# Kernel optimization log

Hardware: AMD Instinct MI355X
Metric: run time of the kernel (lower is better)

Reference implementation:

```python
import jax, jax.numpy as jnp
import numpy as np

B, IMG, TXT = 1, 2048, 256
D_MODEL = 2048
HEADS, HEAD_DIM = 16, 128
INNER = HEADS * HEAD_DIM
EPS = 1e-5
SCALE = HEAD_DIM ** -0.5


def _rmsnorm(x, w):
    # normalize over last dim (head_dim)
    return (x * jax.lax.rsqrt(jnp.mean(x * x, axis=-1, keepdims=True) + EPS)) * w


def _rope(x, cos, sin):
    # x: (B, S, H, D); cos/sin: (S, D) with pairwise-repeated freqs (interleaved convention)
    c = cos[None, :, None, :]
    s = sin[None, :, None, :]
    x1 = x[..., 0::2]
    x2 = x[..., 1::2]
    rot = jnp.stack([-x2, x1], axis=-1).reshape(x.shape)
    return x * c + rot * s


def setup_inputs() -> dict:
    key = jax.random.key(0)
    ks = jax.random.split(key, 12)
    sc_in = D_MODEL ** -0.5
    sc_inner = INNER ** -0.5
    inp = {
        'hidden_states': jax.random.normal(ks[0], (B, IMG, D_MODEL), jnp.float32),
        'encoder_hidden_states': jax.random.normal(ks[1], (B, TXT, D_MODEL), jnp.float32),
    }
    # RoPE tables over the joint (text + image) sequence, interleaved pair layout
    pos = jnp.arange(TXT + IMG, dtype=jnp.float32)
    inv = 1.0 / (10000.0 ** (jnp.arange(0, HEAD_DIM, 2, dtype=jnp.float32) / HEAD_DIM))
    freqs = pos[:, None] * inv[None, :]
    freqs = jnp.repeat(freqs, 2, axis=-1)  # (S, HEAD_DIM)
    inp['freqs_cos'] = jnp.cos(freqs)
    inp['freqs_sin'] = jnp.sin(freqs)
    # parameters (stored (in, out))
    inp['Wqkv'] = jax.random.normal(ks[2], (D_MODEL, 3 * INNER), jnp.float32) * sc_in
    inp['Wqkv_add'] = jax.random.normal(ks[3], (D_MODEL, 3 * INNER), jnp.float32) * sc_in
    inp['b_qkv_add'] = jax.random.normal(ks[4], (3 * INNER,), jnp.float32) * 0.01
    inp['norm_q_w'] = jnp.ones((HEAD_DIM,), jnp.float32)
    inp['norm_k_w'] = jnp.ones((HEAD_DIM,), jnp.float32)
    inp['norm_aq_w'] = jnp.ones((HEAD_DIM,), jnp.float32)
    inp['norm_ak_w'] = jnp.ones((HEAD_DIM,), jnp.float32)
    inp['Wout'] = jax.random.normal(ks[5], (INNER, D_MODEL), jnp.float32) * sc_inner
    inp['b_out'] = jax.random.normal(ks[6], (D_MODEL,), jnp.float32) * 0.01
    inp['Wadd_out'] = jax.random.normal(ks[7], (INNER, D_MODEL), jnp.float32) * sc_inner
    inp['b_add_out'] = jax.random.normal(ks[8], (D_MODEL,), jnp.float32) * 0.01
    return inp


def reference(hidden_states, encoder_hidden_states, freqs_cos, freqs_sin,
              Wqkv, Wqkv_add, b_qkv_add, norm_q_w, norm_k_w, norm_aq_w, norm_ak_w,
              Wout, b_out, Wadd_out, b_add_out):
    b, s_img, _ = hidden_states.shape
    s_txt = encoder_hidden_states.shape[1]

    # fused QKV projection (image stream), chunk q/k/v, unflatten heads
    qkv = hidden_states @ Wqkv  # (B, IMG, 3*INNER)
    q, k, v = jnp.split(qkv, 3, axis=-1)
    q = _rmsnorm(q.reshape(b, s_img, HEADS, HEAD_DIM), norm_q_w)
    k = _rmsnorm(k.reshape(b, s_img, HEADS, HEAD_DIM), norm_k_w)
    v = v.reshape(b, s_img, HEADS, HEAD_DIM)

    # fused QKV projection (text stream, with bias)
    eqkv = encoder_hidden_states @ Wqkv_add + b_qkv_add
    eq, ek, ev = jnp.split(eqkv, 3, axis=-1)
    eq = _rmsnorm(eq.reshape(b, s_txt, HEADS, HEAD_DIM), norm_aq_w)
    ek = _rmsnorm(ek.reshape(b, s_txt, HEADS, HEAD_DIM), norm_ak_w)
    ev = ev.reshape(b, s_txt, HEADS, HEAD_DIM)

    # joint [text; image] concatenation, then RoPE on joint Q/K
    jq = jnp.concatenate([eq, q], axis=1)
    jk = jnp.concatenate([ek, k], axis=1)
    jv = jnp.concatenate([ev, v], axis=1)
    jq = _rope(jq, freqs_cos, freqs_sin)
    jk = _rope(jk, freqs_cos, freqs_sin)

    # non-causal scaled dot-product attention, layout (B, S, H, D)
    scores = jnp.einsum('bqhd,bkhd->bhqk', jq, jk) * SCALE
    probs = jax.nn.softmax(scores, axis=-1)
    out = jnp.einsum('bhqk,bkhd->bqhd', probs, jv)  # (B, S_joint, H, D)
    out = out.reshape(b, s_txt + s_img, INNER)

    enc_out = out[:, :s_txt]
    img_out = out[:, s_txt:]
    img_out = img_out @ Wout + b_out
    enc_out = enc_out @ Wadd_out + b_add_out
    return (img_out, enc_out)
```

## Files before the change

### kernel.cpp

```cpp
#include <hip/hip_runtime.h>
#include <stdint.h>

#define HEADS 16
#define HD 128
#define S_TXT 256
#define S_IMG 2048
#define S_ALL 2304
#define DMODEL 2048
#define N_QKV 6144
#define INNER 2048
#define ATT_EPS 1e-5f
#define ATT_SCALE 0.08838834764831845f
#define LOG2E 1.4426950408889634f
#define MBOUND 16.5f
#define QT_N 18
#define TPS 18

typedef __attribute__((ext_vector_type(8))) __bf16 bf16x8;
typedef __attribute__((ext_vector_type(4))) float f32x4;
typedef __attribute__((ext_vector_type(4))) uint32_t u32x4;

__device__ __forceinline__ uint16_t f2bf(float f) {
  union { float f; uint32_t u; } v; v.f = f;
  uint32_t r = (v.u + 0x7FFF + ((v.u >> 16) & 1)) >> 16;
  return (uint16_t)r;
}
__device__ __forceinline__ float bf2f(uint16_t h) {
  union { float f; uint32_t u; } v; v.u = ((uint32_t)h) << 16;
  return v.f;
}
__device__ __forceinline__ uint32_t cvt_pk_bf16(float lo, float hi) {
  uint32_t r;
  asm("v_cvt_pk_bf16_f32 %0, %1, %2" : "=v"(r) : "v"(lo), "v"(hi));
  return r;
}
__device__ __forceinline__ float fexp2(float x) {
#if __has_builtin(__builtin_amdgcn_exp2f)
  return __builtin_amdgcn_exp2f(x);
#else
  return __expf(x * 0.69314718055994531f);
#endif
}

__device__ __forceinline__ void async_cp16(const void* g, void* l) {
  __builtin_amdgcn_global_load_lds(
      (const __attribute__((address_space(1))) void*)g,
      (__attribute__((address_space(3))) void*)l, 16, 0, 0);
}

__global__ __launch_bounds__(256) void k_cvt2(
    const float* __restrict__ s0, uint16_t* __restrict__ d0, int n40,
    const float* __restrict__ s1, uint16_t* __restrict__ d1, int n41) {
  const float* src; uint16_t* dst; int n4, bid, nb;
  if (blockIdx.x < 1024) { src = s0; dst = d0; n4 = n40; bid = blockIdx.x; nb = 1024; }
  else { src = s1; dst = d1; n4 = n41; bid = blockIdx.x - 1024; nb = 128; }
  int i = bid * 256 + threadIdx.x;
  int stride = nb * 256;
  for (; i < n4; i += stride) {
    float4 v = ((const float4*)src)[i];
    uint2 o;
    o.x = cvt_pk_bf16(v.x, v.y);
    o.y = cvt_pk_bf16(v.z, v.w);
    ((uint2*)dst)[i] = o;
  }
}

__global__ __launch_bounds__(256) void k_cvt_t4(
    const float* __restrict__ s0, uint16_t* __restrict__ d0,
    const float* __restrict__ s1, uint16_t* __restrict__ d1,
    const float* __restrict__ s2, uint16_t* __restrict__ d2,
    const float* __restrict__ s3, uint16_t* __restrict__ d3) {
  __shared__ float t[64][65];
  int b = blockIdx.x;
  const float* src; uint16_t* dst; int R, C, tb;
  if (b < 3072)      { src = s0; dst = d0; R = DMODEL; C = N_QKV;  tb = b; }
  else if (b < 6144) { src = s1; dst = d1; R = DMODEL; C = N_QKV;  tb = b - 3072; }
  else if (b < 7168) { src = s2; dst = d2; R = INNER;  C = DMODEL; tb = b - 6144; }
  else               { src = s3; dst = d3; R = INNER;  C = DMODEL; tb = b - 7168; }
  int ntr = R >> 6;
  int tr = tb % ntr, tc = tb / ntr;
  int tid = threadIdx.x;
  int rr = tid >> 4, c4 = (tid & 15) * 4;
#pragma unroll
  for (int j = 0; j < 4; ++j) {
    int r = rr + j * 16;
    float4 v = *(const float4*)&src[(size_t)(tr * 64 + r) * C + tc * 64 + c4];
    *(float4*)&t[r][c4] = v;
  }
  __syncthreads();
  int cc = tid >> 4, r4 = (tid & 15) * 4;
#pragma unroll
  for (int j = 0; j < 4; ++j) {
    int c = cc + j * 16;
    uint2 o;
    o.x = cvt_pk_bf16(t[r4 + 0][c], t[r4 + 1][c]);
    o.y = cvt_pk_bf16(t[r4 + 2][c], t[r4 + 3][c]);
    *(uint2*)&dst[(size_t)(tc * 64 + c) * R + tr * 64 + r4] = o;
  }
}

__global__ __launch_bounds__(512, 1) void k_gemm2(
    const uint16_t* __restrict__ A0, const uint16_t* __restrict__ B0,
    const float* __restrict__ bias0, uint16_t* __restrict__ C0,
    const uint16_t* __restrict__ A1, const uint16_t* __restrict__ B1,
    const float* __restrict__ bias1, uint16_t* __restrict__ C1,
    int seg0_tiles, int N, int K) {
  __shared__ __align__(16) char lds[2 * 65536];
  int bn = blockIdx.x, bm = blockIdx.y;
  const uint16_t* A; const uint16_t* B; const float* bias; uint16_t* C; int mrow;
  if (bm < seg0_tiles) { A = A0; B = B0; bias = bias0; C = C0; mrow = bm * 256; }
  else { A = A1; B = B1; bias = bias1; C = C1; mrow = (bm - seg0_tiles) * 256; }
  int tid = threadIdx.x, lane = tid & 63, w = tid >> 6;
  int g = lane >> 4, li = lane & 15;
  int wm = w >> 2, wn = w & 3;
  const int NKI = K / 64;

  int rowin = lane >> 3;
  int csrc = (lane & 7) ^ rowin;

  auto stage = [&](int t, char* buf) {
    int kt = t * 64;
#pragma unroll
    for (int j = 0; j < 4; ++j) {
      int r = w * 4 + j;
      int tr = r * 8 + rowin;
      async_cp16(A + (size_t)(mrow + tr) * K + kt + 8 * csrc, buf + r * 1024);
    }
#pragma unroll
    for (int j = 0; j < 4; ++j) {
      int r = w * 4 + j;
      int tr = r * 8 + rowin;
      async_cp16(B + (size_t)(bn * 256 + tr) * K + kt + 8 * csrc, buf + 32768 + r * 1024);
    }
  };

  f32x4 acc[8][4] = {};

  stage(0, lds);
  asm volatile("s_waitcnt vmcnt(0)" ::: "memory");
  __builtin_amdgcn_s_barrier();
  asm volatile("" ::: "memory");

  for (int t = 0; t < NKI; ++t) {
    const char* cur = lds + (t & 1) * 65536;
    if (t + 1 < NKI) stage(t + 1, lds + ((t + 1) & 1) * 65536);

#pragma unroll
    for (int kk = 0; kk < 2; ++kk) {
      bf16x8 af[8], bfv[4];
#pragma unroll
      for (int mi = 0; mi < 8; ++mi) {
        int row = wm * 128 + mi * 16 + li;
        int ch = (kk * 4 + g) ^ (row & 7);
        af[mi] = __builtin_bit_cast(bf16x8, *(const u32x4*)(cur + row * 128 + ch * 16));
      }
#pragma unroll
      for (int ni = 0; ni < 4; ++ni) {
        int row = wn * 64 + ni * 16 + li;
        int ch = (kk * 4 + g) ^ (row & 7);
        bfv[ni] = __builtin_bit_cast(bf16x8, *(const u32x4*)(cur + 32768 + row * 128 + ch * 16));
      }
      __builtin_amdgcn_s_setprio(1);
#pragma unroll
      for (int mi = 0; mi < 8; ++mi)
#pragma unroll
        for (int ni = 0; ni < 4; ++ni)
          acc[mi][ni] = __builtin_amdgcn_mfma_f32_16x16x32_bf16(af[mi], bfv[ni], acc[mi][ni], 0, 0, 0);
      __builtin_amdgcn_s_setprio(0);
    }

    if (t + 1 < NKI) {
      asm volatile("s_waitcnt vmcnt(0)" ::: "memory");
      __builtin_amdgcn_s_barrier();
      asm volatile("" ::: "memory");
    }
  }

#pragma unroll
  for (int mi = 0; mi < 8; ++mi) {
#pragma unroll
    for (int ni = 0; ni < 4; ++ni) {
      int col = bn * 256 + wn * 64 + ni * 16 + li;
      float bv = bias ? bias[col] : 0.0f;
#pragma unroll
      for (int i = 0; i < 4; ++i) {
        int r = mrow + wm * 128 + mi * 16 + 4 * g + i;
        C[(size_t)r * N + col] = f2bf(acc[mi][ni][i] + bv);
      }
    }
  }
}

__global__ __launch_bounds__(256, 4) void k_gemmO(
    const uint16_t* __restrict__ A0, const uint16_t* __restrict__ B0,
    const float* __restrict__ bias0, float* __restrict__ C0,
    const uint16_t* __restrict__ A1, const uint16_t* __restrict__ B1,
    const float* __restrict__ bias1, float* __restrict__ C1,
    int seg0_tiles, int N, int K) {
  __shared__ __align__(16) char lds[4 * 8192];
  int bn = blockIdx.x, bm = blockIdx.y;
  const uint16_t* A; const uint16_t* B; const float* bias; float* C; int mrow;
  if (bm < seg0_tiles) { A = A0; B = B0; bias = bias0; C = C0; mrow = bm * 128; }
  else { A = A1; B = B1; bias = bias1; C = C1; mrow = (bm - seg0_tiles) * 128; }
  int tid = threadIdx.x, lane = tid & 63, w = tid >> 6;
  int g = lane >> 4, li = lane & 15;
  int wm = w >> 1, wn = w & 1;
  const int NKT = K / 32;

  int rowin = lane >> 2;
  int csrc = (lane & 3) ^ (rowin & 3);

  auto stage = [&](int t, int buf) {
    int kt = t * 32;
#pragma unroll
    for (int j = 0; j < 2; ++j) {
      int r = w * 2 + j;
      int tr = r * 16 + rowin;
      async_cp16(A + (size_t)(mrow + tr) * K + kt + 8 * csrc, lds + buf * 8192 + r * 1024);
    }
#pragma unroll
    for (int j = 0; j < 2; ++j) {
      int r = w * 2 + j;
      int tr = r * 16 + rowin;
      async_cp16(B + (size_t)(bn * 128 + tr) * K + kt + 8 * csrc, lds + 16384 + buf * 8192 + r * 1024);
    }
  };

  f32x4 acc[4][4] = {};
  stage(0, 0);
  asm volatile("s_waitcnt vmcnt(0)" ::: "memory");
  __builtin_amdgcn_s_barrier();
  asm volatile("" ::: "memory");

  for (int t = 0; t < NKT; ++t) {
    int cur = t & 1;
    bool pre = (t + 1 < NKT);
    if (pre) stage(t + 1, cur ^ 1);
    const char* Ac = lds + cur * 8192;
    const char* Bc = lds + 16384 + cur * 8192;

    bf16x8 af[4], bfv[4];
#pragma unroll
    for (int mi = 0; mi < 4; ++mi) {
      int row = wm * 64 + mi * 16 + li;
      af[mi] = __builtin_bit_cast(bf16x8, *(const u32x4*)(Ac + row * 64 + (g ^ (row & 3)) * 16));
    }
#pragma unroll
    for (int ni = 0; ni < 4; ++ni) {
      int row = wn * 64 + ni * 16 + li;
      bfv[ni] = __builtin_bit_cast(bf16x8, *(const u32x4*)(Bc + row * 64 + (g ^ (row & 3)) * 16));
    }
    __builtin_amdgcn_s_setprio(1);
#pragma unroll
    for (int mi = 0; mi < 4; ++mi)
#pragma unroll
      for (int ni = 0; ni < 4; ++ni)
        acc[mi][ni] = __builtin_amdgcn_mfma_f32_16x16x32_bf16(af[mi], bfv[ni], acc[mi][ni], 0, 0, 0);
    __builtin_amdgcn_s_setprio(0);

    if (pre) asm volatile("s_waitcnt vmcnt(0)" ::: "memory");
    __builtin_amdgcn_s_barrier();
    asm volatile("" ::: "memory");
  }

#pragma unroll
  for (int mi = 0; mi < 4; ++mi) {
#pragma unroll
    for (int ni = 0; ni < 4; ++ni) {
      int col = bn * 128 + wn * 64 + ni * 16 + li;
      float bv = bias[col];
#pragma unroll
      for (int i = 0; i < 4; ++i) {
        int r = mrow + wm * 64 + mi * 16 + 4 * g + i;
        C[(size_t)r * N + col] = acc[mi][ni][i] + bv;
      }
    }
  }
}

__global__ __launch_bounds__(256) void k_postvt(
    const uint16_t* __restrict__ qkv_img, const uint16_t* __restrict__ qkv_txt,
    const float* __restrict__ fcos, const float* __restrict__ fsin,
    const float* __restrict__ wq, const float* __restrict__ wk,
    const float* __restrict__ waq, const float* __restrict__ wak,
    uint16_t* __restrict__ Qo, uint16_t* __restrict__ Ko, uint16_t* __restrict__ VTo) {
  __shared__ uint16_t Vl[64][136];
  if (blockIdx.x < S_ALL) {
    int s = blockIdx.x;
    const uint16_t* row = (s < S_TXT) ? qkv_txt + (size_t)s * N_QKV
                                      : qkv_img + (size_t)(s - S_TXT) * N_QKV;
    const float* wqp = (s < S_TXT) ? waq : wq;
    const float* wkp = (s < S_TXT) ? wak : wk;
    int lane = threadIdx.x & 63, w = threadIdx.x >> 6;
    int h = w * 4 + (lane >> 4);
    int d0 = (lane & 15) * 8;
    float cs[8], sn[8];
#pragma unroll
    for (int j = 0; j < 8; ++j) {
      cs[j] = fcos[s * HD + d0 + j];
      sn[j] = fsin[s * HD + d0 + j];
    }
#pragma unroll
    for (int part = 0; part < 2; ++part) {
      const uint16_t* src = row + part * INNER + h * HD + d0;
      u32x4 raw = *(const u32x4*)src;
      const uint16_t* rp = (const uint16_t*)&raw;
      float x[8], ss = 0.f;
#pragma unroll
      for (int j = 0; j < 8; ++j) { x[j] = bf2f(rp[j]); ss += x[j] * x[j]; }
      ss += __shfl_xor(ss, 1); ss += __shfl_xor(ss, 2);
      ss += __shfl_xor(ss, 4); ss += __shfl_xor(ss, 8);
      float rn = rsqrtf(ss * (1.0f / HD) + ATT_EPS);
      const float* wp = part ? wkp : wqp;
#pragma unroll
      for (int j = 0; j < 8; ++j) x[j] = x[j] * rn * wp[d0 + j];
      float y[8];
#pragma unroll
      for (int j = 0; j < 8; j += 2) {
        y[j]     = x[j] * cs[j] - x[j + 1] * sn[j];
        y[j + 1] = x[j + 1] * cs[j + 1] + x[j] * sn[j + 1];
      }
      float sc = part ? 1.0f : (ATT_SCALE * LOG2E);
      uint16_t ov[8];
#pragma unroll
      for (int j = 0; j < 8; ++j) ov[j] = f2bf(y[j] * sc);
      uint16_t* dst = (part ? Ko : Qo) + ((size_t)h * S_ALL + s) * HD + d0;
      *(u32x4*)dst = *(const u32x4*)ov;
    }
  } else {
    int b = blockIdx.x - S_ALL;
    int st = b % 36, h = b / 36;
    int s0 = st * 64;
    const uint16_t* base = (s0 < S_TXT) ? qkv_txt + (size_t)s0 * N_QKV
                                        : qkv_img + (size_t)(s0 - S_TXT) * N_QKV;
    base += 2 * INNER + h * HD;
    int tid = threadIdx.x;
#pragma unroll
    for (int it = 0; it < 4; ++it) {
      int idx = it * 256 + tid;
      int r = idx >> 4, c = idx & 15;
      *(u32x4*)&Vl[r][c * 8] = *(const u32x4*)(base + (size_t)r * N_QKV + c * 8);
    }
    __syncthreads();
#pragma unroll
    for (int it = 0; it < 4; ++it) {
      int idx = it * 256 + tid;
      int d = idx >> 3, sc = (idx & 7) * 8;
      uint16_t tmp[8];
#pragma unroll
      for (int j = 0; j < 8; ++j) tmp[j] = Vl[sc + j][d];
      *(u32x4*)&VTo[((size_t)h * HD + d) * S_ALL + s0 + sc] = *(const u32x4*)tmp;
    }
  }
}

__global__ __launch_bounds__(256, 3) void k_attn(
    const uint16_t* __restrict__ Qg, const uint16_t* __restrict__ Kg,
    const uint16_t* __restrict__ VTg,
    uint16_t* __restrict__ part0, uint16_t* __restrict__ part1,
    uint16_t* __restrict__ part2, uint16_t* __restrict__ part3,
    float* __restrict__ lsumP) {
  __shared__ __align__(16) char Kt[2][8192];
  __shared__ __align__(16) char Vt[2][8192];
  __shared__ __align__(16) uint16_t Pl[4][32 * 40];

  int b0 = blockIdx.x;
  int bid = (b0 & 7) * 144 + (b0 >> 3);
  int h = bid / 72, r6 = bid % 72, sp = r6 / 18, qt = r6 % 18;
  int tid = threadIdx.x, lane = tid & 63, w = tid >> 6;
  int g = lane >> 4, li = lane & 15;

  const uint16_t* Kh = Kg + (size_t)h * S_ALL * HD;
  const uint16_t* Vh = VTg + (size_t)h * HD * S_ALL;
  uint16_t* po = (sp & 2) ? ((sp & 1) ? part3 : part2) : ((sp & 1) ? part1 : part0);
  po += ((size_t)(h * QT_N + qt) * 128 + w * 32) * 128;

  int qbase = qt * 128 + w * 32;
  bf16x8 qf[2][4];
#pragma unroll
  for (int q2 = 0; q2 < 2; ++q2) {
    const uint16_t* qp = Qg + ((size_t)h * S_ALL + qbase + q2 * 16 + li) * HD;
#pragma unroll
    for (int kc = 0; kc < 4; ++kc)
      qf[q2][kc] = __builtin_bit_cast(bf16x8, *(const u32x4*)(qp + kc * 32 + g * 8));
  }
  f32x4 o[2][8] = {};
  float lsum[2] = {0.f, 0.f};

  auto stage = [&](int tk, int buf) {
#pragma unroll
    for (int j = 0; j < 2; ++j) {
      int cj = w * 128 + j * 64 + lane;
      int row = cj >> 4, c = (cj & 15) ^ (row & 15);
      async_cp16(Kh + (size_t)(tk * 32 + row) * HD + 8 * c, Kt[buf] + (w * 128 + j * 64) * 16);
    }
#pragma unroll
    for (int j = 0; j < 2; ++j) {
      int cj = w * 128 + j * 64 + lane;
      int row = cj >> 2, c = (cj & 3) ^ ((row >> 1) & 3);
      async_cp16(Vh + (size_t)row * S_ALL + tk * 32 + 8 * c, Vt[buf] + (w * 128 + j * 64) * 16);
    }
  };

  int t0 = sp * TPS;
  stage(t0, 0);
  asm volatile("s_waitcnt vmcnt(0)" ::: "memory");
  __builtin_amdgcn_s_barrier();
  asm volatile("" ::: "memory");

  for (int t = 0; t < TPS; ++t) {
    int cur = t & 1;
    if (t + 1 < TPS) stage(t0 + t + 1, cur ^ 1);
    const char* KtC = Kt[cur];
    const char* VtC = Vt[cur];

    f32x4 sc[2][2];
#pragma unroll
    for (int q2 = 0; q2 < 2; ++q2)
#pragma unroll
      for (int kb = 0; kb < 2; ++kb)
        sc[q2][kb] = (f32x4){-MBOUND, -MBOUND, -MBOUND, -MBOUND};
    __builtin_amdgcn_s_setprio(1);
#pragma unroll
    for (int kb = 0; kb < 2; ++kb)
#pragma unroll
      for (int kc = 0; kc < 4; ++kc) {
        int ch = (kc * 4 + g) ^ li;
        bf16x8 kf = __builtin_bit_cast(bf16x8,
            *(const u32x4*)(KtC + (kb * 16 + li) * 256 + ch * 16));
        sc[0][kb] = __builtin_amdgcn_mfma_f32_16x16x32_bf16(kf, qf[0][kc], sc[0][kb], 0, 0, 0);
        sc[1][kb] = __builtin_amdgcn_mfma_f32_16x16x32_bf16(kf, qf[1][kc], sc[1][kb], 0, 0, 0);
      }
    __builtin_amdgcn_s_setprio(0);

    uint16_t* Pw = &Pl[w][0];
#pragma unroll
    for (int q2 = 0; q2 < 2; ++q2)
#pragma unroll
      for (int kb = 0; kb < 2; ++kb) {
        float p0 = fexp2(sc[q2][kb][0]);
        float p1 = fexp2(sc[q2][kb][1]);
        float p2 = fexp2(sc[q2][kb][2]);
        float p3 = fexp2(sc[q2][kb][3]);
        lsum[q2] += (p0 + p1) + (p2 + p3);
        uint2 pk;
        pk.x = cvt_pk_bf16(p0, p1);
        pk.y = cvt_pk_bf16(p2, p3);
        *(uint2*)((char*)Pw + (q2 * 16 + li) * 80 + kb * 32 + g * 8) = pk;
      }

    bf16x8 pf[2];
#pragma unroll
    for (int q2 = 0; q2 < 2; ++q2)
      pf[q2] = __builtin_bit_cast(bf16x8,
          *(const u32x4*)((const char*)Pw + (q2 * 16 + li) * 80 + g * 16));
    __builtin_amdgcn_s_setprio(1);
#pragma unroll
    for (int db = 0; db < 8; ++db) {
      int vrow = db * 16 + li;
      int ch = g ^ ((vrow >> 1) & 3);
      bf16x8 vf = __builtin_bit_cast(bf16x8, *(const u32x4*)(VtC + vrow * 64 + ch * 16));
      o[0][db] = __builtin_amdgcn_mfma_f32_16x16x32_bf16(pf[0], vf, o[0][db], 0, 0, 0);
      o[1][db] = __builtin_amdgcn_mfma_f32_16x16x32_bf16(pf[1], vf, o[1][db], 0, 0, 0);
    }
    __builtin_amdgcn_s_setprio(0);

    asm volatile("s_waitcnt vmcnt(0)" ::: "memory");
    __builtin_amdgcn_s_barrier();
    asm volatile("" ::: "memory");
  }

#pragma unroll
  for (int q2 = 0; q2 < 2; ++q2) {
    float v = lsum[q2];
    v += __shfl_xor(v, 16);
    v += __shfl_xor(v, 32);
    lsum[q2] = v;
  }
  if (lane < 16) {
#pragma unroll
    for (int q2 = 0; q2 < 2; ++q2)
      lsumP[((size_t)sp * HEADS + h) * S_ALL + qbase + q2 * 16 + lane] = lsum[q2];
  }
#pragma unroll
  for (int q2 = 0; q2 < 2; ++q2)
#pragma unroll
    for (int db = 0; db < 8; ++db)
#pragma unroll
      for (int i = 0; i < 4; ++i)
        po[(q2 * 16 + 4 * g + i) * 128 + db * 16 + li] = f2bf(o[q2][db][i]);
}

__global__ __launch_bounds__(256) void k_comb(
    const uint16_t* __restrict__ p0, const uint16_t* __restrict__ p1,
    const uint16_t* __restrict__ p2, const uint16_t* __restrict__ p3,
    const float* __restrict__ lsumP, uint16_t* __restrict__ attn) {
  int q = blockIdx.x, qt = q >> 7, ql = q & 127;
#pragma unroll
  for (int rep = 0; rep < 2; ++rep) {
    int d4 = threadIdx.x + rep * 256;
    int d = d4 * 4, h = d >> 7, dl = d & 127;
    size_t off = (((size_t)h * QT_N + qt) * 128 + ql) * 128 + dl;
    uint2 a = *(const uint2*)&p0[off];
    uint2 b = *(const uint2*)&p1[off];
    uint2 c = *(const uint2*)&p2[off];
    uint2 e = *(const uint2*)&p3[off];
    const uint16_t* ap = (const uint16_t*)&a;
    const uint16_t* bp = (const uint16_t*)&b;
    const uint16_t* cp = (const uint16_t*)&c;
    const uint16_t* ep = (const uint16_t*)&e;
    float l = 0.f;
#pragma unroll
    for (int s = 0; s < 4; ++s)
      l += lsumP[((size_t)s * HEADS + h) * S_ALL + q];
    float inv = 1.0f / l;
    uint16_t ov[4];
#pragma unroll
    for (int j = 0; j < 4; ++j)
      ov[j] = f2bf((bf2f(ap[j]) + bf2f(bp[j]) + bf2f(cp[j]) + bf2f(ep[j])) * inv);
    *(uint2*)&attn[(size_t)q * INNER + d] = *(const uint2*)ov;
  }
}

extern "C" void kernel_launch(void* const* d_in, const int* in_sizes, int n_in,
                              void* d_out, int out_size, void* d_ws, size_t ws_size,
                              hipStream_t stream) {
  const float* hidden = (const float*)d_in[0];
  const float* enc    = (const float*)d_in[1];
  const float* fcos   = (const float*)d_in[2];
  const float* fsin   = (const float*)d_in[3];
  const float* Wqkv   = (const float*)d_in[4];
  const float* Wqkva  = (const float*)d_in[5];
  const float* bqkva  = (const float*)d_in[6];
  const float* nqw    = (const float*)d_in[7];
  const float* nkw    = (const float*)d_in[8];
  const float* naqw   = (const float*)d_in[9];
  const float* nakw   = (const float*)d_in[10];
  const float* Wout   = (const float*)d_in[11];
  const float* bout   = (const float*)d_in[12];
  const float* Wadd   = (const float*)d_in[13];
  const float* badd   = (const float*)d_in[14];
  float* out_img = (float*)d_out;
  float* out_enc = (float*)d_out + (size_t)S_IMG * DMODEL;

  char* ws = (char*)d_ws;
  size_t off = 0;
  auto alloc = [&](size_t bytes) {
    char* p = ws + off;
    off += (bytes + 255) & ~(size_t)255;
    return p;
  };
  uint16_t* hs_bf   = (uint16_t*)alloc((size_t)S_IMG * DMODEL * 2);
  uint16_t* enc_bf  = (uint16_t*)alloc((size_t)S_TXT * DMODEL * 2);
  char*     wqkv_base = alloc((size_t)N_QKV * DMODEL * 2 * 2);
  uint16_t* WqkvT   = (uint16_t*)wqkv_base;
  uint16_t* WqkvaT  = (uint16_t*)(wqkv_base + (size_t)N_QKV * DMODEL * 2);
  uint16_t* WoutT   = (uint16_t*)alloc((size_t)DMODEL * INNER * 2);
  uint16_t* WaddT   = (uint16_t*)alloc((size_t)DMODEL * INNER * 2);
  uint16_t* qkv_img = (uint16_t*)alloc((size_t)S_IMG * N_QKV * 2);
  uint16_t* qkv_txt = (uint16_t*)alloc((size_t)S_TXT * N_QKV * 2);
  uint16_t* Qb   = (uint16_t*)wqkv_base;
  uint16_t* Kb   = Qb + (size_t)HEADS * S_ALL * HD;
  uint16_t* VTb  = Kb + (size_t)HEADS * S_ALL * HD;
  uint16_t* attn = VTb + (size_t)HEADS * S_ALL * HD;
  uint16_t* part0 = (uint16_t*)d_out;
  uint16_t* part1 = part0 + (size_t)S_ALL * INNER;
  uint16_t* part2 = (uint16_t*)qkv_img;
  uint16_t* part3 = part2 + (size_t)S_ALL * INNER;
  float* lsumP = (float*)enc_bf;

  k_cvt2<<<1152, 256, 0, stream>>>(hidden, hs_bf, S_IMG * DMODEL / 4,
                                   enc, enc_bf, S_TXT * DMODEL / 4);
  k_cvt_t4<<<8192, 256, 0, stream>>>(Wqkv, WqkvT, Wqkva, WqkvaT, Wout, WoutT, Wadd, WaddT);

  dim3 gq(N_QKV / 256, (S_TXT + S_IMG) / 256);
  k_gemm2<<<gq, 512, 0, stream>>>(enc_bf, WqkvaT, bqkva, qkv_txt,
                                  hs_bf, WqkvT, nullptr, qkv_img,
                                  1, N_QKV, DMODEL);

  k_postvt<<<S_ALL + 36 * HEADS, 256, 0, stream>>>(qkv_img, qkv_txt, fcos, fsin,
                                                   nqw, nkw, naqw, nakw, Qb, Kb, VTb);

  k_attn<<<HEADS * QT_N * 4, 256, 0, stream>>>(Qb, Kb, VTb, part0, part1, part2, part3, lsumP);
  k_comb<<<S_ALL, 256, 0, stream>>>(part0, part1, part2, part3, lsumP, attn);

  dim3 go(DMODEL / 128, S_ALL / 128);
  k_gemmO<<<go, 256, 0, stream>>>(attn, WaddT, badd, out_enc,
                                  attn + (size_t)S_TXT * INNER, WoutT, bout, out_img,
                                  2, DMODEL, DMODEL);
}
```

Baseline: 211.5 us.

## Triple-buffer GEMM LDS stages with two-ahead prefetch interleaved into MFMA

Both the QKV GEMM and the output GEMM move from double buffering to a three-stage LDS ring that prefetches two K-tiles ahead. A and B loads are split and issued between the two halves of the MFMA block, and a partial vmcnt wait replaces the full drain. The QKV GEMM also shrinks its K tile from 64 to 32 and changes its swizzle to fit. The aim is to hide global-load latency behind compute, at the cost of more barriers per unit of K and, for gemmO, lower occupancy from the larger LDS footprint.

```diff
diff --git a/kernel.cpp b/kernel.cpp
--- a/kernel.cpp
+++ b/kernel.cpp
@@ -105,7 +105,7 @@
     const uint16_t* __restrict__ A1, const uint16_t* __restrict__ B1,
     const float* __restrict__ bias1, uint16_t* __restrict__ C1,
     int seg0_tiles, int N, int K) {
-  __shared__ __align__(16) char lds[2 * 65536];
+  __shared__ __align__(16) char lds[3 * 32768];
   int bn = blockIdx.x, bm = blockIdx.y;
   const uint16_t* A; const uint16_t* B; const float* bias; uint16_t* C; int mrow;
   if (bm < seg0_tiles) { A = A0; B = B0; bias = bias0; C = C0; mrow = bm * 256; }
@@ -113,64 +113,78 @@
   int tid = threadIdx.x, lane = tid & 63, w = tid >> 6;
   int g = lane >> 4, li = lane & 15;
   int wm = w >> 2, wn = w & 3;
-  const int NKI = K / 64;
-
-  int rowin = lane >> 3;
-  int csrc = (lane & 7) ^ rowin;
-
-  auto stage = [&](int t, char* buf) {
-    int kt = t * 64;
-#pragma unroll
-    for (int j = 0; j < 4; ++j) {
-      int r = w * 4 + j;
-      int tr = r * 8 + rowin;
+  const int NKI = K / 32;
+
+  int rowin = lane >> 2;
+  int csrc = (lane & 3) ^ ((rowin >> 1) & 3);
+
+  auto stageA = [&](int t, char* buf) {
+    int kt = t * 32;
+#pragma unroll
+    for (int j = 0; j < 2; ++j) {
+      int r = w * 2 + j;
+      int tr = r * 16 + rowin;
       async_cp16(A + (size_t)(mrow + tr) * K + kt + 8 * csrc, buf + r * 1024);
     }
-#pragma unroll
-    for (int j = 0; j < 4; ++j) {
-      int r = w * 4 + j;
-      int tr = r * 8 + rowin;
-      async_cp16(B + (size_t)(bn * 256 + tr) * K + kt + 8 * csrc, buf + 32768 + r * 1024);
-    }
   };
+  auto stageB = [&](int t, char* buf) {
+    int kt = t * 32;
+#pragma unroll
+    for (int j = 0; j < 2; ++j) {
+      int r = w * 2 + j;
+      int tr = r * 16 + rowin;
+      async_cp16(B + (size_t)(bn * 256 + tr) * K + kt + 8 * csrc, buf + 16384 + r * 1024);
+    }
+  };
 
   f32x4 acc[8][4] = {};
 
-  stage(0, lds);
-  asm volatile("s_waitcnt vmcnt(0)" ::: "memory");
+  stageA(0, lds); stageB(0, lds);
+  stageA(1, lds + 32768); stageB(1, lds + 32768);
+  asm volatile("s_waitcnt vmcnt(4)" ::: "memory");
   __builtin_amdgcn_s_barrier();
   asm volatile("" ::: "memory");
 
   for (int t = 0; t < NKI; ++t) {
-    const char* cur = lds + (t & 1) * 65536;
-    if (t + 1 < NKI) stage(t + 1, lds + ((t + 1) & 1) * 65536);
-
-#pragma unroll
-    for (int kk = 0; kk < 2; ++kk) {
-      bf16x8 af[8], bfv[4];
-#pragma unroll
-      for (int mi = 0; mi < 8; ++mi) {
-        int row = wm * 128 + mi * 16 + li;
-        int ch = (kk * 4 + g) ^ (row & 7);
-        af[mi] = __builtin_bit_cast(bf16x8, *(const u32x4*)(cur + row * 128 + ch * 16));
-      }
-#pragma unroll
-      for (int ni = 0; ni < 4; ++ni) {
-        int row = wn * 64 + ni * 16 + li;
-        int ch = (kk * 4 + g) ^ (row & 7);
-        bfv[ni] = __builtin_bit_cast(bf16x8, *(const u32x4*)(cur + 32768 + row * 128 + ch * 16));
-      }
-      __builtin_amdgcn_s_setprio(1);
-#pragma unroll
-      for (int mi = 0; mi < 8; ++mi)
-#pragma unroll
-        for (int ni = 0; ni < 4; ++ni)
-          acc[mi][ni] = __builtin_amdgcn_mfma_f32_16x16x32_bf16(af[mi], bfv[ni], acc[mi][ni], 0, 0, 0);
-      __builtin_amdgcn_s_setprio(0);
-    }
+    const char* cur = lds + (t % 3) * 32768;
+    char* nxt = lds + ((t + 2) % 3) * 32768;
+    bool pre = (t + 2 < NKI);
+
+    bf16x8 af[8], bfv[4];
+#pragma unroll
+    for (int mi = 0; mi < 8; ++mi) {
+      int row = wm * 128 + mi * 16 + li;
+      int ch = g ^ ((row >> 1) & 3);
+      af[mi] = __builtin_bit_cast(bf16x8, *(const u32x4*)(cur + row * 64 + ch * 16));
+    }
+#pragma unroll
+    for (int ni = 0; ni < 4; ++ni) {
+      int row = wn * 64 + ni * 16 + li;
+      int ch = g ^ ((row >> 1) & 3);
+      bfv[ni] = __builtin_bit_cast(bf16x8, *(const u32x4*)(cur + 16384 + row * 64 + ch * 16));
+    }
+
+    if (pre) stageA(t + 2, nxt);
+    __builtin_amdgcn_s_setprio(1);
+#pragma unroll
+    for (int mi = 0; mi < 4; ++mi)
+#pragma unroll
+      for (int ni = 0; ni < 4; ++ni)
+        acc[mi][ni] = __builtin_amdgcn_mfma_f32_16x16x32_bf16(af[mi], bfv[ni], acc[mi][ni], 0, 0, 0);
+    __builtin_amdgcn_s_setprio(0);
+
+    if (pre) stageB(t + 2, nxt);
+    __builtin_amdgcn_s_setprio(1);
+#pragma unroll
+    for (int mi = 4; mi < 8; ++mi)
+#pragma unroll
+      for (int ni = 0; ni < 4; ++ni)
+        acc[mi][ni] = __builtin_amdgcn_mfma_f32_16x16x32_bf16(af[mi], bfv[ni], acc[mi][ni], 0, 0, 0);
+    __builtin_amdgcn_s_setprio(0);
 
     if (t + 1 < NKI) {
-      asm volatile("s_waitcnt vmcnt(0)" ::: "memory");
+      if (pre) asm volatile("s_waitcnt vmcnt(4)" ::: "memory");
+      else     asm volatile("s_waitcnt vmcnt(0)" ::: "memory");
       __builtin_amdgcn_s_barrier();
       asm volatile("" ::: "memory");
     }
@@ -191,13 +205,13 @@
   }
 }
 
-__global__ __launch_bounds__(256, 4) void k_gemmO(
+__global__ __launch_bounds__(256, 3) void k_gemmO(
     const uint16_t* __restrict__ A0, const uint16_t* __restrict__ B0,
     const float* __restrict__ bias0, float* __restrict__ C0,
     const uint16_t* __restrict__ A1, const uint16_t* __restrict__ B1,
     const float* __restrict__ bias1, float* __restrict__ C1,
     int seg0_tiles, int N, int K) {
-  __shared__ __align__(16) char lds[4 * 8192];
+  __shared__ __align__(16) char lds[3 * 16384];
   int bn = blockIdx.x, bm = blockIdx.y;
   const uint16_t* A; const uint16_t* B; const float* bias; float* C; int mrow;
   if (bm < seg0_tiles) { A = A0; B = B0; bias = bias0; C = C0; mrow = bm * 128; }
@@ -210,57 +224,73 @@
   int rowin = lane >> 2;
   int csrc = (lane & 3) ^ (rowin & 3);
 
-  auto stage = [&](int t, int buf) {
+  auto stageA = [&](int t, char* buf) {
     int kt = t * 32;
 #pragma unroll
     for (int j = 0; j < 2; ++j) {
       int r = w * 2 + j;
       int tr = r * 16 + rowin;
-      async_cp16(A + (size_t)(mrow + tr) * K + kt + 8 * csrc, lds + buf * 8192 + r * 1024);
-    }
+      async_cp16(A + (size_t)(mrow + tr) * K + kt + 8 * csrc, buf + r * 1024);
+    }
+  };
+  auto stageB = [&](int t, char* buf) {
+    int kt = t * 32;
 #pragma unroll
     for (int j = 0; j < 2; ++j) {
       int r = w * 2 + j;
       int tr = r * 16 + rowin;
-      async_cp16(B + (size_t)(bn * 128 + tr) * K + kt + 8 * csrc, lds + 16384 + buf * 8192 + r * 1024);
+      async_cp16(B + (size_t)(bn * 128 + tr) * K + kt + 8 * csrc, buf + 8192 + r * 1024);
     }
   };
 
   f32x4 acc[4][4] = {};
-  stage(0, 0);
-  asm volatile("s_waitcnt vmcnt(0)" ::: "memory");
+  stageA(0, lds); stageB(0, lds);
+  stageA(1, lds + 16384); stageB(1, lds + 16384);
+  asm volatile("s_waitcnt vmcnt(4)" ::: "memory");
   __builtin_amdgcn_s_barrier();
   asm volatile("" ::: "memory");
 
   for (int t = 0; t < NKT; ++t) {
-    int cur = t & 1;
-    bool pre = (t + 1 < NKT);
-    if (pre) stage(t + 1, cur ^ 1);
-    const char* Ac = lds + cur * 8192;
-    const char* Bc = lds + 16384 + cur * 8192;
+    const char* cur = lds + (t % 3) * 16384;
+    char* nxt = lds + ((t + 2) % 3) * 16384;
+    bool pre = (t + 2 < NKT);
 
     bf16x8 af[4], bfv[4];
 #pragma unroll
     for (int mi = 0; mi < 4; ++mi) {
       int row = wm * 64 + mi * 16 + li;
-      af[mi] = __builtin_bit_cast(bf16x8, *(const u32x4*)(Ac + row * 64 + (g ^ (row & 3)) * 16));
+      af[mi] = __builtin_bit_cast(bf16x8, *(const u32x4*)(cur + row * 64 + (g ^ (row & 3)) * 16));
     }
 #pragma unroll
     for (int ni = 0; ni < 4; ++ni) {
       int row = wn * 64 + ni * 16 + li;
-      bfv[ni] = __builtin_bit_cast(bf16x8, *(const u32x4*)(Bc + row * 64 + (g ^ (row & 3)) * 16));
-    }
+      bfv[ni] = __builtin_bit_cast(bf16x8, *(const u32x4*)(cur + 8192 + row * 64 + (g ^ (row & 3)) * 16));
+    }
+
+    if (pre) stageA(t + 2, nxt);
     __builtin_amdgcn_s_setprio(1);
 #pragma unroll
-    for (int mi = 0; mi < 4; ++mi)
+    for (int mi = 0; mi < 2; ++mi)
 #pragma unroll
       for (int ni = 0; ni < 4; ++ni)
         acc[mi][ni] = __builtin_amdgcn_mfma_f32_16x16x32_bf16(af[mi], bfv[ni], acc[mi][ni], 0, 0, 0);
     __builtin_amdgcn_s_setprio(0);
 
-    if (pre) asm volatile("s_waitcnt vmcnt(0)" ::: "memory");
-    __builtin_amdgcn_s_barrier();
-    asm volatile("" ::: "memory");
+    if (pre) stageB(t + 2, nxt);
+    __builtin_amdgcn_s_setprio(1);
+#pragma unroll
+    for (int mi = 2; mi < 4; ++mi)
+#pragma unroll
+      for (int ni = 0; ni < 4; ++ni)
+        acc[mi][ni] = __builtin_amdgcn_mfma_f32_16x16x32_bf16(af[mi], bfv[ni], acc[mi][ni], 0, 0, 0);
+    __builtin_amdgcn_s_setprio(0);
+
+    if (t + 1 < NKT) {
+      if (pre) asm volatile("s_waitcnt vmcnt(4)" ::: "memory");
+      else     asm volatile("s_waitcnt vmcnt(0)" ::: "memory");
+      __builtin_amdgcn_s_barrier();
+      asm volatile("" ::: "memory");
+    }
   }
 
 #pragma unroll
```

Result: no change. 214.1 us (+1.2%).

## Switch attention to 32x32x16 MFMA and keep P in registers via permlane32 swap

Applied to the files above, without the earlier changes.

Rewrites the attention inner loop to use 32x32x16 bf16 MFMA tiles instead of 16x16x32. The softmax probabilities are repacked in registers with v_permlane32_swap into the A-operand layout, which removes the per-wave LDS round trip for P and its shared buffer. With less shared memory and a different register footprint, launch bounds are raised to 4 blocks per SIMD. The risk is register pressure under the tighter occupancy bound, and the register remap of output rows is error-prone.

```diff
diff --git a/kernel.cpp b/kernel.cpp
--- a/kernel.cpp
+++ b/kernel.cpp
@@ -18,6 +18,7 @@
 
 typedef __attribute__((ext_vector_type(8))) __bf16 bf16x8;
 typedef __attribute__((ext_vector_type(4))) float f32x4;
+typedef __attribute__((ext_vector_type(16))) float f32x16;
 typedef __attribute__((ext_vector_type(4))) uint32_t u32x4;
 
 __device__ __forceinline__ uint16_t f2bf(float f) {
@@ -354,7 +355,7 @@
   }
 }
 
-__global__ __launch_bounds__(256, 3) void k_attn(
+__global__ __launch_bounds__(256, 4) void k_attn(
     const uint16_t* __restrict__ Qg, const uint16_t* __restrict__ Kg,
     const uint16_t* __restrict__ VTg,
     uint16_t* __restrict__ part0, uint16_t* __restrict__ part1,
@@ -362,13 +363,12 @@
     float* __restrict__ lsumP) {
   __shared__ __align__(16) char Kt[2][8192];
   __shared__ __align__(16) char Vt[2][8192];
-  __shared__ __align__(16) uint16_t Pl[4][32 * 40];
 
   int b0 = blockIdx.x;
   int bid = (b0 & 7) * 144 + (b0 >> 3);
   int h = bid / 72, r6 = bid % 72, sp = r6 / 18, qt = r6 % 18;
   int tid = threadIdx.x, lane = tid & 63, w = tid >> 6;
-  int g = lane >> 4, li = lane & 15;
+  int hi5 = lane >> 5, l31 = lane & 31;
 
   const uint16_t* Kh = Kg + (size_t)h * S_ALL * HD;
   const uint16_t* Vh = VTg + (size_t)h * HD * S_ALL;
@@ -376,16 +376,15 @@
   po += ((size_t)(h * QT_N + qt) * 128 + w * 32) * 128;
 
   int qbase = qt * 128 + w * 32;
-  bf16x8 qf[2][4];
-#pragma unroll
-  for (int q2 = 0; q2 < 2; ++q2) {
-    const uint16_t* qp = Qg + ((size_t)h * S_ALL + qbase + q2 * 16 + li) * HD;
-#pragma unroll
-    for (int kc = 0; kc < 4; ++kc)
-      qf[q2][kc] = __builtin_bit_cast(bf16x8, *(const u32x4*)(qp + kc * 32 + g * 8));
-  }
-  f32x4 o[2][8] = {};
-  float lsum[2] = {0.f, 0.f};
+  bf16x8 qf[8];
+  {
+    const uint16_t* qp = Qg + ((size_t)h * S_ALL + qbase + l31) * HD + hi5 * 8;
+#pragma unroll
+    for (int s = 0; s < 8; ++s)
+      qf[s] = __builtin_bit_cast(bf16x8, *(const u32x4*)(qp + s * 16));
+  }
+  f32x16 o[4] = {};
+  float lsum = 0.f;
 
   auto stage = [&](int tk, int buf) {
 #pragma unroll
@@ -414,54 +413,52 @@
     const char* KtC = Kt[cur];
     const char* VtC = Vt[cur];
 
-    f32x4 sc[2][2];
-#pragma unroll
-    for (int q2 = 0; q2 < 2; ++q2)
-#pragma unroll
-      for (int kb = 0; kb < 2; ++kb)
-        sc[q2][kb] = (f32x4){-MBOUND, -MBOUND, -MBOUND, -MBOUND};
+    f32x16 sc;
+#pragma unroll
+    for (int r = 0; r < 16; ++r) sc[r] = -MBOUND;
     __builtin_amdgcn_s_setprio(1);
 #pragma unroll
-    for (int kb = 0; kb < 2; ++kb)
-#pragma unroll
-      for (int kc = 0; kc < 4; ++kc) {
-        int ch = (kc * 4 + g) ^ li;
-        bf16x8 kf = __builtin_bit_cast(bf16x8,
-            *(const u32x4*)(KtC + (kb * 16 + li) * 256 + ch * 16));
-        sc[0][kb] = __builtin_amdgcn_mfma_f32_16x16x32_bf16(kf, qf[0][kc], sc[0][kb], 0, 0, 0);
-        sc[1][kb] = __builtin_amdgcn_mfma_f32_16x16x32_bf16(kf, qf[1][kc], sc[1][kb], 0, 0, 0);
-      }
+    for (int s = 0; s < 8; ++s) {
+      int ch = (s * 2 + hi5) ^ (l31 & 15);
+      bf16x8 kf = __builtin_bit_cast(bf16x8, *(const u32x4*)(KtC + l31 * 256 + ch * 16));
+      sc = __builtin_amdgcn_mfma_f32_32x32x16_bf16(kf, qf[s], sc, 0, 0, 0);
+    }
     __builtin_amdgcn_s_setprio(0);
 
-    uint16_t* Pw = &Pl[w][0];
-#pragma unroll
-    for (int q2 = 0; q2 < 2; ++q2)
-#pragma unroll
-      for (int kb = 0; kb < 2; ++kb) {
-        float p0 = fexp2(sc[q2][kb][0]);
-        float p1 = fexp2(sc[q2][kb][1]);
-        float p2 = fexp2(sc[q2][kb][2]);
-        float p3 = fexp2(sc[q2][kb][3]);
-        lsum[q2] += (p0 + p1) + (p2 + p3);
-        uint2 pk;
-        pk.x = cvt_pk_bf16(p0, p1);
-        pk.y = cvt_pk_bf16(p2, p3);
-        *(uint2*)((char*)Pw + (q2 * 16 + li) * 80 + kb * 32 + g * 8) = pk;
-      }
-
-    bf16x8 pf[2];
-#pragma unroll
-    for (int q2 = 0; q2 < 2; ++q2)
-      pf[q2] = __builtin_bit_cast(bf16x8,
-          *(const u32x4*)((const char*)Pw + (q2 * 16 + li) * 80 + g * 16));
+    float p[16];
+#pragma unroll
+    for (int r = 0; r < 16; ++r) p[r] = fexp2(sc[r]);
+#pragma unroll
+    for (int r = 0; r < 16; ++r) lsum += p[r];
+    uint32_t pk0 = cvt_pk_bf16(p[0], p[1]);
+    uint32_t pk1 = cvt_pk_bf16(p[2], p[3]);
+    uint32_t pk2 = cvt_pk_bf16(p[4], p[5]);
+    uint32_t pk3 = cvt_pk_bf16(p[6], p[7]);
+    uint32_t pk4 = cvt_pk_bf16(p[8], p[9]);
+    uint32_t pk5 = cvt_pk_bf16(p[10], p[11]);
+    uint32_t pk6 = cvt_pk_bf16(p[12], p[13]);
+    uint32_t pk7 = cvt_pk_bf16(p[14], p[15]);
+    asm volatile("v_permlane32_swap_b32 %0, %1" : "+v"(pk0), "+v"(pk2));
+    asm volatile("v_permlane32_swap_b32 %0, %1" : "+v"(pk1), "+v"(pk3));
+    asm volatile("v_permlane32_swap_b32 %0, %1" : "+v"(pk4), "+v"(pk6));
+    asm volatile("v_permlane32_swap_b32 %0, %1" : "+v"(pk5), "+v"(pk7));
+    bf16x8 pa0 = __builtin_bit_cast(bf16x8, (u32x4){pk0, pk1, pk2, pk3});
+    bf16x8 pa1 = __builtin_bit_cast(bf16x8, (u32x4){pk4, pk5, pk6, pk7});
+
     __builtin_amdgcn_s_setprio(1);
 #pragma unroll
-    for (int db = 0; db < 8; ++db) {
-      int vrow = db * 16 + li;
-      int ch = g ^ ((vrow >> 1) & 3);
-      bf16x8 vf = __builtin_bit_cast(bf16x8, *(const u32x4*)(VtC + vrow * 64 + ch * 16));
-      o[0][db] = __builtin_amdgcn_mfma_f32_16x16x32_bf16(pf[0], vf, o[0][db], 0, 0, 0);
-      o[1][db] = __builtin_amdgcn_mfma_f32_16x16x32_bf16(pf[1], vf, o[1][db], 0, 0, 0);
+    for (int db = 0; db < 4; ++db) {
+      int d = db * 32 + l31;
+      {
+        int ch = (0 * 2 + hi5) ^ ((d >> 1) & 3);
+        bf16x8 vf = __builtin_bit_cast(bf16x8, *(const u32x4*)(VtC + d * 64 + ch * 16));
+        o[db] = __builtin_amdgcn_mfma_f32_32x32x16_bf16(pa0, vf, o[db], 0, 0, 0);
+      }
+      {
+        int ch = (1 * 2 + hi5) ^ ((d >> 1) & 3);
+        bf16x8 vf = __builtin_bit_cast(bf16x8, *(const u32x4*)(VtC + d * 64 + ch * 16));
+        o[db] = __builtin_amdgcn_mfma_f32_32x32x16_bf16(pa1, vf, o[db], 0, 0, 0);
+      }
     }
     __builtin_amdgcn_s_setprio(0);
 
@@ -470,25 +467,17 @@
     asm volatile("" ::: "memory");
   }
 
-#pragma unroll
-  for (int q2 = 0; q2 < 2; ++q2) {
-    float v = lsum[q2];
-    v += __shfl_xor(v, 16);
-    v += __shfl_xor(v, 32);
-    lsum[q2] = v;
-  }
-  if (lane < 16) {
-#pragma unroll
-    for (int q2 = 0; q2 < 2; ++q2)
-      lsumP[((size_t)sp * HEADS + h) * S_ALL + qbase + q2 * 16 + lane] = lsum[q2];
-  }
-#pragma unroll
-  for (int q2 = 0; q2 < 2; ++q2)
-#pragma unroll
-    for (int db = 0; db < 8; ++db)
-#pragma unroll
-      for (int i = 0; i < 4; ++i)
-        po[(q2 * 16 + 4 * g + i) * 128 + db * 16 + li] = f2bf(o[q2][db][i]);
+  lsum += __shfl_xor(lsum, 32);
+  if (lane < 32)
+    lsumP[((size_t)sp * HEADS + h) * S_ALL + qbase + lane] = lsum;
+
+#pragma unroll
+  for (int db = 0; db < 4; ++db)
+#pragma unroll
+    for (int r = 0; r < 16; ++r) {
+      int q = (r & 3) + 8 * (r >> 2) + 4 * hi5;
+      po[q * 128 + db * 32 + l31] = f2bf(o[db][r]);
+    }
 }
 
 __global__ __launch_bounds__(256) void k_comb(
```

Result: slower. 324.8 us (+53.6%).
